# Optimization experiments

Measured on AMD Instinct MI355X. Metric: run time of the kernel, lower is better.

The kernel has to match this reference:

```python
import jax, jax.numpy as jnp
import numpy as np

N_HEADS = 16
EMBED_DIM = 1024
HEAD_DIM = EMBED_DIM // N_HEADS
SEQ_LEN = 2048


def setup_inputs() -> dict:
    key = jax.random.key(0)
    ks = jax.random.split(key, 9)
    s = 1.0 / np.sqrt(EMBED_DIM)
    inp = {
        "x": jax.random.normal(ks[0], (SEQ_LEN, EMBED_DIM), dtype=jnp.float32),
        "Wq": jax.random.uniform(ks[1], (EMBED_DIM, EMBED_DIM), jnp.float32, -s, s),
        "bq": jax.random.uniform(ks[2], (EMBED_DIM,), jnp.float32, -s, s),
        "Wk": jax.random.uniform(ks[3], (EMBED_DIM, EMBED_DIM), jnp.float32, -s, s),
        "bk": jax.random.uniform(ks[4], (EMBED_DIM,), jnp.float32, -s, s),
        "Wv": jax.random.uniform(ks[5], (EMBED_DIM, EMBED_DIM), jnp.float32, -s, s),
        "bv": jax.random.uniform(ks[6], (EMBED_DIM,), jnp.float32, -s, s),
        "Wo": jax.random.uniform(ks[7], (EMBED_DIM, EMBED_DIM), jnp.float32, -s, s),
        "bo": jax.random.uniform(ks[8], (EMBED_DIM,), jnp.float32, -s, s),
    }
    return inp


def reference(x, Wq, bq, Wk, bk, Wv, bv, Wo, bo):
    # Linear layers (torch convention: y = x @ W.T + b)
    Q = x @ Wq.T + bq  # [S, E]
    K = x @ Wk.T + bk
    V = x @ Wv.T + bv
    # split heads -> [H, S, D]
    def split(t):
        return t.reshape(SEQ_LEN, N_HEADS, HEAD_DIM).transpose(1, 0, 2)
    Qh, Kh, Vh = split(Q), split(K), split(V)
    # NOTE: faithful to source, scale is sqrt(embed_dim), not sqrt(head_dim)
    scale = 1.0 / np.sqrt(EMBED_DIM)
    scores = jnp.einsum("hsd,htd->hst", Qh, Kh) * scale  # [H, S, S]
    attn = jax.nn.softmax(scores, axis=-1)
    ctx = jnp.einsum("hst,htd->hsd", attn, Vh)  # [H, S, D]
    ctx = ctx.transpose(1, 0, 2).reshape(SEQ_LEN, EMBED_DIM)
    out = ctx @ Wo.T + bo
    return (out, attn)
```

## Files before the change

### kernel.cpp

```cpp
#include <hip/hip_runtime.h>
#include <hip/hip_bf16.h>
#include <stdint.h>

#define SQL 2048
#define EMB 1024
#define NHD 16
#define HDD 64

typedef __bf16 bf16x8 __attribute__((ext_vector_type(8)));
typedef __bf16 bf16x4 __attribute__((ext_vector_type(4)));
typedef float f32x4 __attribute__((ext_vector_type(4)));
typedef float f32x16 __attribute__((ext_vector_type(16)));

__device__ __forceinline__ f32x4 mfma16(bf16x8 a, bf16x8 b, f32x4 c) {
    return __builtin_amdgcn_mfma_f32_16x16x32_bf16(a, b, c, 0, 0, 0);
}
__device__ __forceinline__ f32x16 mfma32(bf16x8 a, bf16x8 b, f32x16 c) {
    return __builtin_amdgcn_mfma_f32_32x32x16_bf16(a, b, c, 0, 0, 0);
}

__device__ __forceinline__ void gload_lds16(const __bf16* g, __bf16* lds) {
    __builtin_amdgcn_global_load_lds(
        (const __attribute__((address_space(1))) uint32_t*)g,
        (__attribute__((address_space(3))) uint32_t*)lds,
        16, 0, 0);
}

__global__ void cast5_kernel(const float* __restrict__ x, const float* __restrict__ wq,
                             const float* __restrict__ wk, const float* __restrict__ wv,
                             const float* __restrict__ wo, __bf16* __restrict__ out)
{
    int i = blockIdx.x * blockDim.x + threadIdx.x;
    const float* src; int off;
    if      (i < (512 << 10))  { src = x;  off = 0; }
    else if (i < (768 << 10))  { src = wq; off = 512 << 10; }
    else if (i < (1024 << 10)) { src = wk; off = 768 << 10; }
    else if (i < (1280 << 10)) { src = wv; off = 1024 << 10; }
    else                       { src = wo; off = 1280 << 10; }
    float4 v = ((const float4*)src)[i - off];
    bf16x4 o;
    o[0] = (__bf16)v.x; o[1] = (__bf16)v.y; o[2] = (__bf16)v.z; o[3] = (__bf16)v.w;
    ((bf16x4*)out)[i] = o;
}

template<bool OUT_BF16, bool TRZ2>
__global__ __launch_bounds__(256, 2)
void gemm_bt(const __bf16* __restrict__ A,
             const __bf16* __restrict__ B0, const __bf16* __restrict__ B1, const __bf16* __restrict__ B2,
             const float* __restrict__ bias0, const float* __restrict__ bias1, const float* __restrict__ bias2,
             void* __restrict__ out0, void* __restrict__ out1, void* __restrict__ out2,
             float s0, float s1, float s2,
             int M, int N, int K)
{
    const __bf16* B = B0; const float* bias = bias0; void* Cout = out0; float cscale = s0;
    if (blockIdx.z == 1) { B = B1; bias = bias1; Cout = out1; cscale = s1; }
    if (blockIdx.z == 2) { B = B2; bias = bias2; Cout = out2; cscale = s2; }

    __shared__ __attribute__((aligned(16))) __bf16 As[128 * 32];
    __shared__ __attribute__((aligned(16))) __bf16 Bs[128 * 32];

    const int tid  = threadIdx.x;
    const int lane = tid & 63;
    const int wave = tid >> 6;
    const int lrow = lane & 15;
    const int quad = lane >> 4;
    const int bm = blockIdx.y * 128;
    const int bn = blockIdx.x * 128;
    const int wm = (wave >> 1) * 64;
    const int wn = (wave & 1) * 64;

    const f32x4 fzero = {0.f, 0.f, 0.f, 0.f};
    f32x4 acc[4][4];
#pragma unroll
    for (int i = 0; i < 4; i++)
#pragma unroll
        for (int j = 0; j < 4; j++) acc[i][j] = fzero;

    const int srow = (lane >> 2);
    const int scol = (lane & 3) * 8;

    for (int k0 = 0; k0 < K; k0 += 32) {
        __syncthreads();
#pragma unroll
        for (int i = 0; i < 2; i++) {
            int rbase = wave * 32 + i * 16;
            gload_lds16(&A[(size_t)(bm + rbase + srow) * K + k0 + scol], &As[rbase * 32]);
            gload_lds16(&B[(size_t)(bn + rbase + srow) * K + k0 + scol], &Bs[rbase * 32]);
        }
        __syncthreads();
        bf16x8 af[4], bfr[4];
#pragma unroll
        for (int i = 0; i < 4; i++) af[i]  = *(const bf16x8*)&As[(wm + i * 16 + lrow) * 32 + quad * 8];
#pragma unroll
        for (int i = 0; i < 4; i++) bfr[i] = *(const bf16x8*)&Bs[(wn + i * 16 + lrow) * 32 + quad * 8];
#pragma unroll
        for (int mi = 0; mi < 4; mi++)
#pragma unroll
            for (int ni = 0; ni < 4; ni++)
                acc[mi][ni] = mfma16(af[mi], bfr[ni], acc[mi][ni]);
    }

    const bool trz = TRZ2 && (blockIdx.z == 2);
#pragma unroll
    for (int mi = 0; mi < 4; mi++) {
        int row = bm + wm + mi * 16 + quad * 4;
#pragma unroll
        for (int ni = 0; ni < 4; ni++) {
            int col = bn + wn + ni * 16 + lrow;
            float bv = bias[col];
            if (trz) {
                bf16x4 t;
#pragma unroll
                for (int r = 0; r < 4; r++) t[r] = (__bf16)((acc[mi][ni][r] + bv) * cscale);
                *(bf16x4*)&((__bf16*)Cout)[(size_t)col * SQL + row] = t;
            } else {
#pragma unroll
                for (int r = 0; r < 4; r++) {
                    float v = (acc[mi][ni][r] + bv) * cscale;
                    if (OUT_BF16) ((__bf16*)Cout)[(size_t)(row + r) * N + col] = (__bf16)v;
                    else          ((float*)Cout)[(size_t)(row + r) * N + col] = v;
                }
            }
        }
    }
}

__global__ __launch_bounds__(256, 2)
void attn_kernel(const __bf16* __restrict__ Qg, const __bf16* __restrict__ Kg,
                 const __bf16* __restrict__ Vt, float* __restrict__ attn,
                 __bf16* __restrict__ ctx)
{
    __shared__ __attribute__((aligned(16))) __bf16 Ks[2][64 * 64];
    __shared__ __attribute__((aligned(16))) __bf16 Vs[2][64 * 64];
    __shared__ __attribute__((aligned(16))) __bf16 Ps[4][32 * 40];
    __shared__ float Lb[4][64];
    __shared__ float Ored[64][66];

    const int tid  = threadIdx.x;
    const int lane = tid & 63;
    const int w    = tid >> 6;
    const int wq   = w & 1;
    const int wk   = w >> 1;
    const int l31  = lane & 31;
    const int hi   = lane >> 5;
    const int h  = blockIdx.y;
    const int q0 = blockIdx.x * 64;

    const f32x16 Z16 = {0.f,0.f,0.f,0.f,0.f,0.f,0.f,0.f,0.f,0.f,0.f,0.f,0.f,0.f,0.f,0.f};

    bf16x8 qf[2][4];
#pragma unroll
    for (int qg = 0; qg < 2; qg++) {
        const __bf16* qp = &Qg[(size_t)(q0 + qg * 32 + l31) * EMB + h * HDD + hi * 8];
#pragma unroll
        for (int ds = 0; ds < 4; ds++) qf[qg][ds] = *(const bf16x8*)&qp[ds * 16];
    }

    {
        const __bf16* kp = &Kg[(size_t)(w * 32 + l31) * EMB + h * HDD + hi * 8];
        const size_t tstep = (size_t)128 * EMB;
        bf16x8 kcur[4], knxt[4];
#pragma unroll
        for (int ds = 0; ds < 4; ds++) kcur[ds] = *(const bf16x8*)&kp[ds * 16];
        float ls0 = 0.f, ls1 = 0.f;
        for (int t = 0; t < 16; t++) {
            if (t < 15) {
#pragma unroll
                for (int ds = 0; ds < 4; ds++)
                    knxt[ds] = *(const bf16x8*)&kp[(size_t)(t + 1) * tstep + ds * 16];
            }
            f32x16 sA = Z16, sB = Z16;
#pragma unroll
            for (int ds = 0; ds < 4; ds++) {
                sA = mfma32(kcur[ds], qf[0][ds], sA);
                sB = mfma32(kcur[ds], qf[1][ds], sB);
            }
#pragma unroll
            for (int r = 0; r < 16; r++) { ls0 += __expf(sA[r]); ls1 += __expf(sB[r]); }
            if (t < 15) {
#pragma unroll
                for (int ds = 0; ds < 4; ds++) kcur[ds] = knxt[ds];
            }
        }
        ls0 += __shfl_xor(ls0, 32);
        ls1 += __shfl_xor(ls1, 32);
        if (hi == 0) { Lb[w][l31] = ls0; Lb[w][32 + l31] = ls1; }
    }

    const int srow  = lane >> 3;
    const int sslot = (lane & 7) ^ (srow & 7);
    auto stageK = [&](int buf, int k0) {
#pragma unroll
        for (int j = 0; j < 2; j++) {
            int r = w * 16 + j * 8;
            gload_lds16(&Kg[(size_t)(k0 + r + srow) * EMB + h * HDD + sslot * 8],
                        &Ks[buf][r * 64]);
        }
    };
    auto stageV = [&](int buf, int k0) {
#pragma unroll
        for (int j = 0; j < 2; j++) {
            int r = w * 16 + j * 8;
            gload_lds16(&Vt[(size_t)(h * HDD + r + srow) * SQL + k0 + sslot * 8],
                        &Vs[buf][r * 64]);
        }
    };

    stageK(0, 0);
    stageV(0, 0);
    __syncthreads();

    float rinv;
    {
        int q = wq * 32 + l31;
        rinv = 1.f / (Lb[0][q] + Lb[1][q] + Lb[2][q] + Lb[3][q]);
    }

    f32x16 o0 = Z16, o1 = Z16;
    float* __restrict__ arow = attn + (size_t)h * SQL * SQL + (size_t)(q0 + wq * 32 + l31) * SQL;
    const int krowoff = (wk * 32 + l31) * 64;
    const int lane7   = lane & 7;
    const int vrow0 = l31 * 64;
    const int vrow1 = (32 + l31) * 64;
    const int psrow = l31 * 40;
    const bf16x8* qfp = qf[wq];

    int buf = 0;
    for (int t = 0; t < 32; t++) {
        const int k0 = t * 64;
        if (t < 31) { stageK(buf ^ 1, k0 + 64); stageV(buf ^ 1, k0 + 64); }
        f32x16 s = Z16;
#pragma unroll
        for (int ds = 0; ds < 4; ds++) {
            bf16x8 kf = *(const bf16x8*)&Ks[buf][krowoff + ((((ds << 1) | hi) ^ lane7) << 3)];
            s = mfma32(kf, qfp[ds], s);
        }
#pragma unroll
        for (int g = 0; g < 4; g++) {
            f32x4 pv; bf16x4 pb;
#pragma unroll
            for (int i = 0; i < 4; i++) {
                float p = __expf(s[g * 4 + i]) * rinv;
                pv[i] = p; pb[i] = (__bf16)p;
            }
            *(f32x4*)&arow[k0 + wk * 32 + g * 8 + hi * 4] = pv;
            *(bf16x4*)&Ps[w][psrow + g * 8 + hi * 4] = pb;
        }
#pragma unroll
        for (int kt = 0; kt < 2; kt++) {
            bf16x8 pf = *(const bf16x8*)&Ps[w][psrow + kt * 16 + hi * 8];
            int vslot = (((wk << 2) | (kt << 1) | hi) ^ lane7) << 3;
            bf16x8 v0 = *(const bf16x8*)&Vs[buf][vrow0 + vslot];
            bf16x8 v1 = *(const bf16x8*)&Vs[buf][vrow1 + vslot];
            o0 = mfma32(v0, pf, o0);
            o1 = mfma32(v1, pf, o1);
        }
        __syncthreads();
        buf ^= 1;
    }

    if (wk == 1) {
#pragma unroll
        for (int g = 0; g < 4; g++)
#pragma unroll
            for (int i = 0; i < 4; i++) {
                int dl = i + g * 8 + hi * 4;
                Ored[dl][wq * 32 + l31]      = o0[g * 4 + i];
                Ored[32 + dl][wq * 32 + l31] = o1[g * 4 + i];
            }
    }
    __syncthreads();
    if (wk == 0) {
        __bf16* crow = &ctx[(size_t)(q0 + wq * 32 + l31) * EMB + h * HDD];
#pragma unroll
        for (int g = 0; g < 4; g++) {
            bf16x4 c0, c1;
#pragma unroll
            for (int i = 0; i < 4; i++) {
                int dl = i + g * 8 + hi * 4;
                c0[i] = (__bf16)(o0[g * 4 + i] + Ored[dl][wq * 32 + l31]);
                c1[i] = (__bf16)(o1[g * 4 + i] + Ored[32 + dl][wq * 32 + l31]);
            }
            *(bf16x4*)&crow[g * 8 + hi * 4]      = c0;
            *(bf16x4*)&crow[32 + g * 8 + hi * 4] = c1;
        }
    }
}

extern "C" void kernel_launch(void* const* d_in, const int* in_sizes, int n_in,
                              void* d_out, int out_size, void* d_ws, size_t ws_size,
                              hipStream_t stream)
{
    const float* x  = (const float*)d_in[0];
    const float* Wq = (const float*)d_in[1];
    const float* bq = (const float*)d_in[2];
    const float* Wk = (const float*)d_in[3];
    const float* bk = (const float*)d_in[4];
    const float* Wv = (const float*)d_in[5];
    const float* bv = (const float*)d_in[6];
    const float* Wo = (const float*)d_in[7];
    const float* bo = (const float*)d_in[8];

    float* out  = (float*)d_out;
    float* attn = out + (size_t)SQL * EMB;

    const size_t M1 = 1u << 20;
    __bf16* wsb = (__bf16*)d_ws;
    __bf16* xb  = wsb;
    __bf16* wqb = wsb + 2 * M1;
    __bf16* wkb = wsb + 3 * M1;
    __bf16* wvb = wsb + 4 * M1;
    __bf16* wob = wsb + 5 * M1;
    __bf16* Qb  = wsb + 6 * M1;
    __bf16* Kb  = wsb + 8 * M1;
    __bf16* Vtb = wsb + 12 * M1;
    __bf16* ctb = wsb + 14 * M1;

    cast5_kernel<<<6144, 256, 0, stream>>>(x, Wq, Wk, Wv, Wo, wsb);

    gemm_bt<true, true><<<dim3(EMB / 128, SQL / 128, 3), 256, 0, stream>>>(
        xb, wqb, wkb, wvb, bq, bk, bv,
        (void*)Qb, (void*)Kb, (void*)Vtb,
        0.03125f, 1.0f, 1.0f, SQL, EMB, EMB);

    attn_kernel<<<dim3(SQL / 64, NHD), 256, 0, stream>>>(Qb, Kb, Vtb, attn, ctb);

    gemm_bt<false, false><<<dim3(EMB / 128, SQL / 128, 1), 256, 0, stream>>>(
        ctb, wob, wob, wob, bo, bo, bo,
        (void*)out, (void*)out, (void*)out,
        1.0f, 1.0f, 1.0f, SQL, EMB, EMB);
}
```

Baseline: 416.7 us.

## Stage attention probabilities in LDS and write coalesced nontemporal rows

The probability tile is now staged as fp32 in a double-buffered shared array instead of each lane writing scattered 16-byte chunks straight to global memory. After the block barrier, all threads read it back and store it as fully coalesced contiguous row segments with nontemporal stores. The bf16 operand for the PV MFMA is converted from that fp32 tile. The cost being targeted is the inefficient strided write of the large attention matrix. In exchange the kernel uses more LDS, which may reduce occupancy, and adds an extra shared-memory round trip per tile.

```diff
diff --git a/kernel.cpp b/kernel.cpp
--- a/kernel.cpp
+++ b/kernel.cpp
@@ -132,9 +132,9 @@
 {
     __shared__ __attribute__((aligned(16))) __bf16 Ks[2][64 * 64];
     __shared__ __attribute__((aligned(16))) __bf16 Vs[2][64 * 64];
-    __shared__ __attribute__((aligned(16))) __bf16 Ps[4][32 * 40];
+    __shared__ __attribute__((aligned(16))) float  Pf[2][64 * 68];
     __shared__ float Lb[4][64];
-    __shared__ float Ored[64][66];
+    float* Ored = &Pf[0][0];
 
     const int tid  = threadIdx.x;
     const int lane = tid & 63;
@@ -217,12 +217,12 @@
     }
 
     f32x16 o0 = Z16, o1 = Z16;
-    float* __restrict__ arow = attn + (size_t)h * SQL * SQL + (size_t)(q0 + wq * 32 + l31) * SQL;
+    float* __restrict__ attn_h = attn + (size_t)h * SQL * SQL;
     const int krowoff = (wk * 32 + l31) * 64;
     const int lane7   = lane & 7;
     const int vrow0 = l31 * 64;
     const int vrow1 = (32 + l31) * 64;
-    const int psrow = l31 * 40;
+    const int pq    = (wq * 32 + l31) * 68;
     const bf16x8* qfp = qf[wq];
 
     int buf = 0;
@@ -237,18 +237,19 @@
         }
 #pragma unroll
         for (int g = 0; g < 4; g++) {
-            f32x4 pv; bf16x4 pb;
-#pragma unroll
-            for (int i = 0; i < 4; i++) {
-                float p = __expf(s[g * 4 + i]) * rinv;
-                pv[i] = p; pb[i] = (__bf16)p;
-            }
-            *(f32x4*)&arow[k0 + wk * 32 + g * 8 + hi * 4] = pv;
-            *(bf16x4*)&Ps[w][psrow + g * 8 + hi * 4] = pb;
+            f32x4 pv;
+#pragma unroll
+            for (int i = 0; i < 4; i++) pv[i] = __expf(s[g * 4 + i]) * rinv;
+            *(f32x4*)&Pf[buf][pq + wk * 32 + g * 8 + hi * 4] = pv;
         }
 #pragma unroll
         for (int kt = 0; kt < 2; kt++) {
-            bf16x8 pf = *(const bf16x8*)&Ps[w][psrow + kt * 16 + hi * 8];
+            const float* pp = &Pf[buf][pq + wk * 32 + kt * 16 + hi * 8];
+            f32x4 pA = *(const f32x4*)pp;
+            f32x4 pB = *(const f32x4*)(pp + 4);
+            bf16x8 pf;
+#pragma unroll
+            for (int i = 0; i < 4; i++) { pf[i] = (__bf16)pA[i]; pf[i + 4] = (__bf16)pB[i]; }
             int vslot = (((wk << 2) | (kt << 1) | hi) ^ lane7) << 3;
             bf16x8 v0 = *(const bf16x8*)&Vs[buf][vrow0 + vslot];
             bf16x8 v1 = *(const bf16x8*)&Vs[buf][vrow1 + vslot];
@@ -256,6 +257,14 @@
             o1 = mfma32(v1, pf, o1);
         }
         __syncthreads();
+#pragma unroll
+        for (int j = 0; j < 4; j++) {
+            int lin = j * 256 + tid;
+            int r   = lin >> 4;
+            int c   = (lin & 15) << 2;
+            f32x4 v = *(const f32x4*)&Pf[buf][r * 68 + c];
+            __builtin_nontemporal_store(v, (f32x4*)&attn_h[(size_t)(q0 + r) * SQL + k0 + c]);
+        }
         buf ^= 1;
     }
 
@@ -265,8 +274,8 @@
 #pragma unroll
             for (int i = 0; i < 4; i++) {
                 int dl = i + g * 8 + hi * 4;
-                Ored[dl][wq * 32 + l31]      = o0[g * 4 + i];
-                Ored[32 + dl][wq * 32 + l31] = o1[g * 4 + i];
+                Ored[dl * 66 + wq * 32 + l31]        = o0[g * 4 + i];
+                Ored[(32 + dl) * 66 + wq * 32 + l31] = o1[g * 4 + i];
             }
     }
     __syncthreads();
@@ -278,8 +287,8 @@
 #pragma unroll
             for (int i = 0; i < 4; i++) {
                 int dl = i + g * 8 + hi * 4;
-                c0[i] = (__bf16)(o0[g * 4 + i] + Ored[dl][wq * 32 + l31]);
-                c1[i] = (__bf16)(o1[g * 4 + i] + Ored[32 + dl][wq * 32 + l31]);
+                c0[i] = (__bf16)(o0[g * 4 + i] + Ored[dl * 66 + wq * 32 + l31]);
+                c1[i] = (__bf16)(o1[g * 4 + i] + Ored[(32 + dl) * 66 + wq * 32 + l31]);
             }
             *(bf16x4*)&crow[g * 8 + hi * 4]      = c0;
             *(bf16x4*)&crow[32 + g * 8 + hi * 4] = c1;
```

Result: no change. 409.8 us (-1.7%).
